# Optimization experiments

Hardware: AMD Instinct MI355X
Metric: run time of the kernel (lower is better)

## Reference

```python
import jax, jax.numpy as jnp
import numpy as np

NUM_HEADS = 8
KERNEL = 3


def _arsinh_norm(x, w, b):
    # ArsinhNorm with scale=1.0: weight * asinh(x) + bias
    return w * jnp.arcsinh(x) + b


def _nbr_idx(L, k):
    # NATTEN neighborhood: window start clamped so the k-window stays in-bounds
    start = jnp.clip(jnp.arange(L) - k // 2, 0, L - k)
    return start[:, None] + jnp.arange(k)  # [L, k]


def _na2d(x, qkv_w, qkv_b, proj_w, proj_b, num_heads=NUM_HEADS, k=KERNEL):
    B, H, W, C = x.shape
    hd = C // num_heads
    qkv = x @ qkv_w + qkv_b                      # [B,H,W,3C]
    q, kk, v = jnp.split(qkv, 3, axis=-1)
    q = q.reshape(B, H, W, num_heads, hd) * (hd ** -0.5)
    kk = kk.reshape(B, H, W, num_heads, hd)
    v = v.reshape(B, H, W, num_heads, hd)
    ri = _nbr_idx(H, k)[:, None, :, None]        # [H,1,k,1]
    ci = _nbr_idx(W, k)[None, :, None, :]        # [1,W,1,k]
    nb_k = kk[:, ri, ci].reshape(B, H, W, k * k, num_heads, hd)  # gather 3x3 neighborhood
    nb_v = v[:, ri, ci].reshape(B, H, W, k * k, num_heads, hd)
    scores = jnp.einsum('bijnd,bijmnd->bijnm', q, nb_k)          # [B,H,W,nh,k*k]
    attn = jax.nn.softmax(scores, axis=-1)
    out = jnp.einsum('bijnm,bijmnd->bijnd', attn, nb_v).reshape(B, H, W, C)
    return out @ proj_w + proj_b


def setup_inputs() -> dict:
    key = jax.random.key(0)
    ks = jax.random.split(key, 8)
    B, H, W, C = 16, 64, 64, 256
    s = 0.02
    return {
        'h': jax.random.normal(ks[0], (B, H, W, C), dtype=jnp.float32),
        'qkv_w': jax.random.normal(ks[1], (C, 3 * C), dtype=jnp.float32) * s,
        'qkv_b': jnp.zeros((3 * C,), jnp.float32),
        'proj_w': jax.random.normal(ks[2], (C, C), dtype=jnp.float32) * s,
        'proj_b': jnp.zeros((C,), jnp.float32),
        'n1_w': jnp.ones((C,), jnp.float32),
        'n1_b': jnp.zeros((C,), jnp.float32),
        'n2_w': jnp.ones((C,), jnp.float32),
        'n2_b': jnp.zeros((C,), jnp.float32),
        'mlp_w1': jax.random.normal(ks[3], (C, 2 * C), dtype=jnp.float32) * s,
        'mlp_b1': jnp.zeros((2 * C,), jnp.float32),
        'mlp_w2': jax.random.normal(ks[4], (2 * C, C), dtype=jnp.float32) * s,
        'mlp_b2': jnp.zeros((C,), jnp.float32),
    }


def reference(h, qkv_w, qkv_b, proj_w, proj_b, n1_w, n1_b, n2_w, n2_b,
              mlp_w1, mlp_b1, mlp_w2, mlp_b2):
    h1 = _arsinh_norm(h, n1_w, n1_b)
    h = h + _na2d(h1, qkv_w, qkv_b, proj_w, proj_b)
    h2 = _arsinh_norm(h, n2_w, n2_b)
    ff = jax.nn.gelu(h2 @ mlp_w1 + mlp_b1, approximate=False) @ mlp_w2 + mlp_b2
    return h + ff
```

## Files before the change

### kernel.cpp

```cpp
#include <hip/hip_runtime.h>
#include <math.h>

typedef unsigned short u16;
typedef unsigned int u32;
typedef __attribute__((ext_vector_type(8))) short short8;
typedef __attribute__((ext_vector_type(4))) float f32x4;

__device__ __forceinline__ float b2f(u16 u) {
    return __uint_as_float(((u32)u) << 16);
}
__device__ __forceinline__ u16 f2b(float f) {
    u32 x = __float_as_uint(f);
    return (u16)((x + 0x7fffu + ((x >> 16) & 1u)) >> 16);
}
__device__ __forceinline__ float ldext(const void* p, size_t i, int isbf) {
    return isbf ? b2f(((const u16*)p)[i]) : ((const float*)p)[i];
}
__device__ __forceinline__ void stext(void* p, size_t i, int isbf, float v) {
    if (isbf) ((u16*)p)[i] = f2b(v);
    else ((float*)p)[i] = v;
}
__device__ __forceinline__ void gl2lds16(const u16* g, u16* l) {
    __builtin_amdgcn_global_load_lds(
        (const __attribute__((address_space(1))) u32*)(const void*)g,
        (__attribute__((address_space(3))) u32*)(void*)l, 16, 0, 0);
}
__device__ __forceinline__ void unpack8(uint4 w, float* f) {
    const u32* pw = (const u32*)&w;
#pragma unroll
    for (int k = 0; k < 4; ++k) {
        f[2 * k]     = __uint_as_float(pw[k] << 16);
        f[2 * k + 1] = __uint_as_float(pw[k] & 0xffff0000u);
    }
}

__global__ void detect_k(const void* __restrict__ h, int* __restrict__ flag) {
    __shared__ int cnt;
    if (threadIdx.x == 0) cnt = 0;
    __syncthreads();
    const u16* p = (const u16*)h;
    int local = 0;
    for (int i = threadIdx.x; i < 4096; i += 256) {
        int e = (p[i] >> 7) & 0xFF;
        if (e != 0 && (e < 110 || e > 133)) local++;
    }
    atomicAdd(&cnt, local);
    __syncthreads();
    if (threadIdx.x == 0) *flag = (cnt < 256) ? 1 : 0;
}

__global__ void transpose_k(const void* __restrict__ src, u16* __restrict__ dst,
                            int R, int C, const int* __restrict__ flag) {
    int isbf = *flag;
    int idx = blockIdx.x * 256 + threadIdx.x;
    if (idx >= R * C) return;
    int r = idx / C, c = idx - r * C;
    dst[c * R + r] = f2b(ldext(src, idx, isbf));
}

__global__ void norm_k(const void* __restrict__ xb, size_t xoff,
                       const void* __restrict__ w, const void* __restrict__ b,
                       u16* __restrict__ y, const int* __restrict__ flag, int force_bf) {
    int isbf = *flag;
    int xisbf = force_bf ? 1 : isbf;
    size_t base = ((size_t)blockIdx.x * 256 + threadIdx.x) * 4;
    int c0 = (int)(base & 255);
    float v[4];
    if (xisbf) {
        uint2 raw = *reinterpret_cast<const uint2*>((const u16*)xb + xoff + base);
        const u16* px = reinterpret_cast<const u16*>(&raw);
#pragma unroll
        for (int j = 0; j < 4; ++j) v[j] = b2f(px[j]);
    } else {
        float4 r = *reinterpret_cast<const float4*>((const float*)xb + xoff + base);
        v[0] = r.x; v[1] = r.y; v[2] = r.z; v[3] = r.w;
    }
    u16 o[4];
#pragma unroll
    for (int j = 0; j < 4; ++j)
        o[j] = f2b(ldext(w, c0 + j, isbf) * asinhf(v[j]) + ldext(b, c0 + j, isbf));
    *reinterpret_cast<uint2*>(y + base) = *reinterpret_cast<uint2*>(o);
}

template <int EPI>
__global__ __launch_bounds__(256) void gemm_bt(
    const u16* __restrict__ A, const u16* __restrict__ BT, const void* __restrict__ bias,
    const void* __restrict__ resb, size_t resoff, void* __restrict__ outb, size_t outoff,
    int N, int K, const int* __restrict__ flag) {
    __shared__ __align__(16) u16 lA[128 * 32];
    __shared__ __align__(16) u16 lB[128 * 32];
    const int isbf = *flag;
    const int tid = threadIdx.x;
    const int lane = tid & 63;
    const int wave = tid >> 6;
    const int waveM = wave >> 1, waveN = wave & 1;
    const int m0 = blockIdx.y * 128;
    const int n0 = blockIdx.x * 128;

    f32x4 acc[4][4];
#pragma unroll
    for (int mi = 0; mi < 4; ++mi)
#pragma unroll
        for (int ni = 0; ni < 4; ++ni)
#pragma unroll
            for (int r = 0; r < 4; ++r) acc[mi][ni][r] = 0.f;

    const int lrow = lane & 15;
    const int ko = (lane >> 4) * 8;

    for (int k0 = 0; k0 < K; k0 += 32) {
        __syncthreads();
#pragma unroll
        for (int q = 0; q < 2; ++q) {
            int s = wave * 2 + q;
            int e0 = (s * 64 + lane) * 8;
            int row = e0 >> 5, col = e0 & 31;
            gl2lds16(&A[(size_t)(m0 + row) * K + k0 + col], &lA[s * 512]);
            gl2lds16(&BT[(size_t)(n0 + row) * K + k0 + col], &lB[s * 512]);
        }
        __syncthreads();
        short8 af[4], bfr[4];
#pragma unroll
        for (int mi = 0; mi < 4; ++mi)
            af[mi] = *reinterpret_cast<const short8*>(&lA[(waveM * 64 + mi * 16 + lrow) * 32 + ko]);
#pragma unroll
        for (int ni = 0; ni < 4; ++ni)
            bfr[ni] = *reinterpret_cast<const short8*>(&lB[(waveN * 64 + ni * 16 + lrow) * 32 + ko]);
#pragma unroll
        for (int mi = 0; mi < 4; ++mi)
#pragma unroll
            for (int ni = 0; ni < 4; ++ni)
                acc[mi][ni] = __builtin_amdgcn_mfma_f32_16x16x32_bf16(af[mi], bfr[ni], acc[mi][ni], 0, 0, 0);
    }

    const int rquad = (lane >> 4) * 4;
    const int ccol = lane & 15;
#pragma unroll
    for (int mi = 0; mi < 4; ++mi)
#pragma unroll
        for (int ni = 0; ni < 4; ++ni) {
            int colg = n0 + waveN * 64 + ni * 16 + ccol;
            float bb = ldext(bias, colg, isbf);
#pragma unroll
            for (int r = 0; r < 4; ++r) {
                int rowg = m0 + waveM * 64 + mi * 16 + rquad + r;
                size_t idx = (size_t)rowg * N + colg;
                float v = acc[mi][ni][r] + bb;
                if (EPI == 0) {
                    ((u16*)outb)[outoff + idx] = f2b(v);
                } else if (EPI == 1) {
                    v = 0.5f * v * (1.f + erff(v * 0.70710678118654752f));
                    ((u16*)outb)[outoff + idx] = f2b(v);
                } else if (EPI == 2) {
                    v += ldext(resb, resoff + idx, isbf);
                    stext(outb, outoff + idx, isbf, v);
                } else if (EPI == 3) {
                    v += ldext(resb, resoff + idx, isbf);
                    ((u16*)outb)[outoff + idx] = f2b(v);
                } else {
                    v += b2f(((const u16*)resb)[resoff + idx]);
                    stext(outb, outoff + idx, isbf, v);
                }
            }
        }
}

__global__ __launch_bounds__(256) void attn_k(const u16* __restrict__ qkv, u16* __restrict__ out) {
    const int t = blockIdx.x * 256 + threadIdx.x;
    const int head = t & 7;
    const int p = t >> 3;
    const int b = p >> 12;
    const int ij = p & 4095;
    const int i = ij >> 6, j = ij & 63;
    int r0 = i - 1; r0 = r0 < 0 ? 0 : (r0 > 61 ? 61 : r0);
    int c0 = j - 1; c0 = c0 < 0 ? 0 : (c0 > 61 ? 61 : c0);

    const u16* qp = qkv + (size_t)p * 768 + head * 32;
    float q[32];
#pragma unroll
    for (int ch = 0; ch < 4; ++ch)
        unpack8(*reinterpret_cast<const uint4*>(qp + ch * 8), q + ch * 8);

    const float qscale = 0.17677669529663687f;
    int nbp[9];
    float sc[9];
#pragma unroll
    for (int dr = 0; dr < 3; ++dr)
#pragma unroll
        for (int dc = 0; dc < 3; ++dc) {
            int nb = dr * 3 + dc;
            int np_ = b * 4096 + (r0 + dr) * 64 + (c0 + dc);
            nbp[nb] = np_;
            const u16* kp = qkv + (size_t)np_ * 768 + 256 + head * 32;
            float dot = 0.f;
#pragma unroll
            for (int ch = 0; ch < 4; ++ch) {
                float kf[8];
                unpack8(*reinterpret_cast<const uint4*>(kp + ch * 8), kf);
#pragma unroll
                for (int e = 0; e < 8; ++e) dot += q[ch * 8 + e] * kf[e];
            }
            sc[nb] = dot * qscale;
        }

    float mx = sc[0];
#pragma unroll
    for (int nb = 1; nb < 9; ++nb) mx = fmaxf(mx, sc[nb]);
    float s = 0.f;
#pragma unroll
    for (int nb = 0; nb < 9; ++nb) { sc[nb] = __expf(sc[nb] - mx); s += sc[nb]; }
    float inv = 1.f / s;

    float acc[32];
#pragma unroll
    for (int e = 0; e < 32; ++e) acc[e] = 0.f;
#pragma unroll
    for (int nb = 0; nb < 9; ++nb) {
        const u16* vp = qkv + (size_t)nbp[nb] * 768 + 512 + head * 32;
        float wgt = sc[nb] * inv;
#pragma unroll
        for (int ch = 0; ch < 4; ++ch) {
            float vf[8];
            unpack8(*reinterpret_cast<const uint4*>(vp + ch * 8), vf);
#pragma unroll
            for (int e = 0; e < 8; ++e) acc[ch * 8 + e] += wgt * vf[e];
        }
    }

    u16 ob[32];
#pragma unroll
    for (int e = 0; e < 32; ++e) ob[e] = f2b(acc[e]);
    uint4* ov = reinterpret_cast<uint4*>(ob);
    uint4* og = reinterpret_cast<uint4*>(out + (size_t)p * 256 + head * 32);
#pragma unroll
    for (int ch = 0; ch < 4; ++ch) og[ch] = ov[ch];
}

extern "C" void kernel_launch(void* const* d_in, const int* in_sizes, int n_in,
                              void* d_out, int out_size, void* d_ws, size_t ws_size,
                              hipStream_t stream) {
    const void* h      = d_in[0];
    const void* qkv_w  = d_in[1];
    const void* qkv_b  = d_in[2];
    const void* proj_w = d_in[3];
    const void* proj_b = d_in[4];
    const void* n1_w   = d_in[5];
    const void* n1_b   = d_in[6];
    const void* n2_w   = d_in[7];
    const void* n2_b   = d_in[8];
    const void* w1     = d_in[9];
    const void* b1     = d_in[10];
    const void* w2     = d_in[11];
    const void* b2     = d_in[12];

    char* ws = (char*)d_ws;
    u16* WqkvT  = (u16*)(ws + 0);
    u16* WprojT = (u16*)(ws + 393216);
    u16* W1T    = (u16*)(ws + 524288);
    u16* W2T    = (u16*)(ws + 786432);
    int* Flag   = (int*)(ws + 1048576);
    char* bufs  = ws + 1049600;

    size_t avail = ws_size > 1049600 ? ws_size - 1049600 : 0;
    int CHUNK = 4096;
    if (avail >= (size_t)65536 * 2048) CHUNK = 65536;
    else if (avail >= (size_t)16384 * 2048) CHUNK = 16384;
    else if (avail >= (size_t)8192 * 2048) CHUNK = 8192;

    u16* H1 = (u16*)bufs;
    u16* S  = (u16*)(bufs + (size_t)CHUNK * 512);

    detect_k<<<1, 256, 0, stream>>>(h, Flag);
    transpose_k<<<768, 256, 0, stream>>>(qkv_w, WqkvT, 256, 768, Flag);
    transpose_k<<<256, 256, 0, stream>>>(proj_w, WprojT, 256, 256, Flag);
    transpose_k<<<512, 256, 0, stream>>>(w1, W1T, 256, 512, Flag);
    transpose_k<<<512, 256, 0, stream>>>(w2, W2T, 512, 256, Flag);

    if (CHUNK == 65536) {
        u16* HNS = S;
        u16* T   = S + (size_t)65536 * 256;
        norm_k<<<16384, 256, 0, stream>>>(h, 0, n1_w, n1_b, H1, Flag, 0);
        { dim3 g(6, 512); gemm_bt<0><<<g, 256, 0, stream>>>(H1, WqkvT, qkv_b, nullptr, 0, S, 0, 768, 256, Flag); }
        attn_k<<<2048, 256, 0, stream>>>(S, H1);
        { dim3 g(2, 512); gemm_bt<3><<<g, 256, 0, stream>>>(H1, WprojT, proj_b, h, 0, HNS, 0, 256, 256, Flag); }
        norm_k<<<16384, 256, 0, stream>>>(HNS, 0, n2_w, n2_b, H1, Flag, 1);
        { dim3 g(4, 512); gemm_bt<1><<<g, 256, 0, stream>>>(H1, W1T, b1, nullptr, 0, T, 0, 512, 256, Flag); }
        { dim3 g(2, 512); gemm_bt<4><<<g, 256, 0, stream>>>(T, W2T, b2, HNS, 0, d_out, 0, 256, 512, Flag); }
    } else {
        const int NCH = 65536 / CHUNK;
        for (int c = 0; c < NCH; ++c) {
            size_t off = (size_t)c * CHUNK * 256;
            norm_k<<<CHUNK / 4, 256, 0, stream>>>(h, off, n1_w, n1_b, H1, Flag, 0);
            { dim3 g(6, CHUNK / 128);
              gemm_bt<0><<<g, 256, 0, stream>>>(H1, WqkvT, qkv_b, nullptr, 0, S, 0, 768, 256, Flag); }
            attn_k<<<CHUNK / 32, 256, 0, stream>>>(S, H1);
            { dim3 g(2, CHUNK / 128);
              gemm_bt<2><<<g, 256, 0, stream>>>(H1, WprojT, proj_b, h, off, d_out, off, 256, 256, Flag); }
        }
        for (int c = 0; c < NCH; ++c) {
            size_t off = (size_t)c * CHUNK * 256;
            norm_k<<<CHUNK / 4, 256, 0, stream>>>(d_out, off, n2_w, n2_b, H1, Flag, 0);
            { dim3 g(4, CHUNK / 128);
              gemm_bt<1><<<g, 256, 0, stream>>>(H1, W1T, b1, nullptr, 0, S, 0, 512, 256, Flag); }
            { dim3 g(2, CHUNK / 128);
              gemm_bt<2><<<g, 256, 0, stream>>>(S, W2T, b2, d_out, off, d_out, off, 256, 512, Flag); }
        }
    }
}
```

Before: 515.4 us.

## Fuse ArsinhNorm into GEMM prologue and keep full-K row tiles resident in LDS

Replaces the separate norm kernels and the K-looped 128x128 GEMM with one GEMM kernel per layer. Each block stages a full 128xK A tile (normalized on the fly for the QKV and MLP1 layers) into XOR-swizzled LDS, then sweeps all N column chunks while reusing that A tile. This removes the norm kernels' write and re-read of activations, cuts per-k-step barriers, and avoids LDS bank conflicts. The cost is 128KB of LDS per block, which limits occupancy to one block per CU, and little overlap between loading B and computing.

```diff
diff --git a/kernel.cpp b/kernel.cpp
--- a/kernel.cpp
+++ b/kernel.cpp
@@ -58,88 +58,60 @@
     dst[c * R + r] = f2b(ldext(src, idx, isbf));
 }
 
-__global__ void norm_k(const void* __restrict__ xb, size_t xoff,
-                       const void* __restrict__ w, const void* __restrict__ b,
-                       u16* __restrict__ y, const int* __restrict__ flag, int force_bf) {
-    int isbf = *flag;
-    int xisbf = force_bf ? 1 : isbf;
-    size_t base = ((size_t)blockIdx.x * 256 + threadIdx.x) * 4;
-    int c0 = (int)(base & 255);
-    float v[4];
-    if (xisbf) {
-        uint2 raw = *reinterpret_cast<const uint2*>((const u16*)xb + xoff + base);
-        const u16* px = reinterpret_cast<const u16*>(&raw);
-#pragma unroll
-        for (int j = 0; j < 4; ++j) v[j] = b2f(px[j]);
-    } else {
-        float4 r = *reinterpret_cast<const float4*>((const float*)xb + xoff + base);
-        v[0] = r.x; v[1] = r.y; v[2] = r.z; v[3] = r.w;
-    }
-    u16 o[4];
-#pragma unroll
-    for (int j = 0; j < 4; ++j)
-        o[j] = f2b(ldext(w, c0 + j, isbf) * asinhf(v[j]) + ldext(b, c0 + j, isbf));
-    *reinterpret_cast<uint2*>(y + base) = *reinterpret_cast<uint2*>(o);
-}
-
-template <int EPI>
-__global__ __launch_bounds__(256) void gemm_bt(
-    const u16* __restrict__ A, const u16* __restrict__ BT, const void* __restrict__ bias,
-    const void* __restrict__ resb, size_t resoff, void* __restrict__ outb, size_t outoff,
-    int N, int K, const int* __restrict__ flag) {
-    __shared__ __align__(16) u16 lA[128 * 32];
-    __shared__ __align__(16) u16 lB[128 * 32];
-    const int isbf = *flag;
-    const int tid = threadIdx.x;
-    const int lane = tid & 63;
+
+template <int K>
+__device__ __forceinline__ void stage_lin(const u16* __restrict__ src, size_t soff,
+                                          int row0, int kcol0, u16* lds, int tid) {
     const int wave = tid >> 6;
-    const int waveM = wave >> 1, waveN = wave & 1;
-    const int m0 = blockIdx.y * 128;
-    const int n0 = blockIdx.x * 128;
-
-    f32x4 acc[4][4];
-#pragma unroll
-    for (int mi = 0; mi < 4; ++mi)
-#pragma unroll
-        for (int ni = 0; ni < 4; ++ni)
-#pragma unroll
-            for (int r = 0; r < 4; ++r) acc[mi][ni][r] = 0.f;
-
+    const int r0 = tid >> 5;
+    const int cbs = ((tid & 31) << 4) ^ (r0 << 4);
+    const u16* s0 = src + soff + (size_t)(row0 + r0) * K + kcol0 + (cbs >> 1);
+#pragma unroll
+    for (int s = 0; s < 16; ++s)
+        gl2lds16(s0 + (size_t)s * 8 * K, lds + s * 2048 + wave * 512);
+}
+
+__device__ __forceinline__ void compute_chunk(const u16* lA, const u16* lB,
+                                              int waveM, int waveN, int lane,
+                                              f32x4 (&acc)[4][4]) {
     const int lrow = lane & 15;
     const int ko = (lane >> 4) * 8;
-
-    for (int k0 = 0; k0 < K; k0 += 32) {
-        __syncthreads();
-#pragma unroll
-        for (int q = 0; q < 2; ++q) {
-            int s = wave * 2 + q;
-            int e0 = (s * 64 + lane) * 8;
-            int row = e0 >> 5, col = e0 & 31;
-            gl2lds16(&A[(size_t)(m0 + row) * K + k0 + col], &lA[s * 512]);
-            gl2lds16(&BT[(size_t)(n0 + row) * K + k0 + col], &lB[s * 512]);
-        }
-        __syncthreads();
+#pragma unroll
+    for (int ks = 0; ks < 8; ++ks) {
         short8 af[4], bfr[4];
-#pragma unroll
-        for (int mi = 0; mi < 4; ++mi)
-            af[mi] = *reinterpret_cast<const short8*>(&lA[(waveM * 64 + mi * 16 + lrow) * 32 + ko]);
-#pragma unroll
-        for (int ni = 0; ni < 4; ++ni)
-            bfr[ni] = *reinterpret_cast<const short8*>(&lB[(waveN * 64 + ni * 16 + lrow) * 32 + ko]);
+        const int kb = (ks * 32 + ko) << 1;
+#pragma unroll
+        for (int mi = 0; mi < 4; ++mi) {
+            int row = waveM * 64 + mi * 16 + lrow;
+            int byte = ((row << 9) + kb) ^ ((row & 7) << 4);
+            af[mi] = *reinterpret_cast<const short8*>(reinterpret_cast<const char*>(lA) + byte);
+        }
+#pragma unroll
+        for (int ni = 0; ni < 4; ++ni) {
+            int row = waveN * 64 + ni * 16 + lrow;
+            int byte = ((row << 9) + kb) ^ ((row & 7) << 4);
+            bfr[ni] = *reinterpret_cast<const short8*>(reinterpret_cast<const char*>(lB) + byte);
+        }
 #pragma unroll
         for (int mi = 0; mi < 4; ++mi)
 #pragma unroll
             for (int ni = 0; ni < 4; ++ni)
                 acc[mi][ni] = __builtin_amdgcn_mfma_f32_16x16x32_bf16(af[mi], bfr[ni], acc[mi][ni], 0, 0, 0);
     }
-
+}
+
+template <int EPI, int N>
+__device__ __forceinline__ void epi_chunk(const f32x4 (&acc)[4][4], int nc, int m0,
+                                          int waveM, int waveN, int lane,
+                                          const void* bias, const void* resb, size_t resoff,
+                                          void* outb, size_t outoff, int isbf) {
     const int rquad = (lane >> 4) * 4;
     const int ccol = lane & 15;
 #pragma unroll
     for (int mi = 0; mi < 4; ++mi)
 #pragma unroll
         for (int ni = 0; ni < 4; ++ni) {
-            int colg = n0 + waveN * 64 + ni * 16 + ccol;
+            int colg = nc * 128 + waveN * 64 + ni * 16 + ccol;
             float bb = ldext(bias, colg, isbf);
 #pragma unroll
             for (int r = 0; r < 4; ++r) {
@@ -165,6 +137,108 @@
         }
 }
 
+template <int PRO, int EPI, int KT, int NC>
+__global__ __launch_bounds__(256) void sgemm(
+    const void* __restrict__ Ax, size_t aoff,
+    const u16* __restrict__ BT,
+    const void* __restrict__ bias,
+    const void* __restrict__ nw, const void* __restrict__ nb,
+    const void* __restrict__ resb, size_t resoff,
+    void* __restrict__ outb, size_t outoff,
+    const int* __restrict__ flag) {
+    static_assert(KT == 1 || (KT == 2 && NC == 2 && PRO == 0), "KT=2 only for MLP2 shape");
+    constexpr int K = KT * 256;
+    constexpr int N = NC * 128;
+    __shared__ __align__(16) u16 lA[128 * 256];
+    __shared__ __align__(16) u16 lB[128 * 256];
+    const int isbf = *flag;
+    const int tid = threadIdx.x;
+    const int lane = tid & 63, wave = tid >> 6;
+    const int waveM = wave >> 1, waveN = wave & 1;
+    const int m0 = blockIdx.x * 128;
+
+    stage_lin<K>(BT, 0, 0, 0, lB, tid);
+
+    if constexpr (PRO == 0) {
+        stage_lin<K>((const u16*)Ax, aoff, m0, 0, lA, tid);
+    } else {
+        const int col = (tid << 2) & 255;
+        const int rb = tid >> 6;
+        float wv[4], bv[4];
+#pragma unroll
+        for (int j = 0; j < 4; ++j) {
+            wv[j] = ldext(nw, col + j, isbf);
+            bv[j] = ldext(nb, col + j, isbf);
+        }
+#pragma unroll 4
+        for (int i = 0; i < 32; ++i) {
+            int row = i * 4 + rb;
+            float v[4];
+            if (PRO == 1 && !isbf) {
+                float4 x = *reinterpret_cast<const float4*>(
+                    (const float*)Ax + aoff + (size_t)(m0 + row) * 256 + col);
+                v[0] = x.x; v[1] = x.y; v[2] = x.z; v[3] = x.w;
+            } else {
+                uint2 xr = *reinterpret_cast<const uint2*>(
+                    (const u16*)Ax + aoff + (size_t)(m0 + row) * 256 + col);
+                const u16* px = reinterpret_cast<const u16*>(&xr);
+#pragma unroll
+                for (int j = 0; j < 4; ++j) v[j] = b2f(px[j]);
+            }
+            u16 o[4];
+#pragma unroll
+            for (int j = 0; j < 4; ++j) o[j] = f2b(wv[j] * asinhf(v[j]) + bv[j]);
+            int byte = ((row << 9) + (col << 1)) ^ ((row & 7) << 4);
+            *reinterpret_cast<uint2*>(reinterpret_cast<char*>(lA) + byte) =
+                *reinterpret_cast<const uint2*>(o);
+        }
+    }
+
+    if constexpr (KT == 1) {
+        __syncthreads();
+        for (int nc = 0; nc < NC; ++nc) {
+            f32x4 acc[4][4];
+#pragma unroll
+            for (int mi = 0; mi < 4; ++mi)
+#pragma unroll
+                for (int ni = 0; ni < 4; ++ni)
+#pragma unroll
+                    for (int r = 0; r < 4; ++r) acc[mi][ni][r] = 0.f;
+            compute_chunk(lA, lB, waveM, waveN, lane, acc);
+            if (nc + 1 < NC) {
+                __syncthreads();
+                stage_lin<K>(BT, 0, (nc + 1) * 128, 0, lB, tid);
+            }
+            epi_chunk<EPI, N>(acc, nc, m0, waveM, waveN, lane, bias,
+                              resb, resoff, outb, outoff, isbf);
+            if (nc + 1 < NC) __syncthreads();
+        }
+    } else {
+        f32x4 acc0[4][4], acc1[4][4];
+#pragma unroll
+        for (int mi = 0; mi < 4; ++mi)
+#pragma unroll
+            for (int ni = 0; ni < 4; ++ni)
+#pragma unroll
+                for (int r = 0; r < 4; ++r) { acc0[mi][ni][r] = 0.f; acc1[mi][ni][r] = 0.f; }
+        for (int kh = 0; kh < 2; ++kh) {
+            if (kh) {
+                __syncthreads();
+                stage_lin<K>(BT, 0, 0, kh * 256, lB, tid);
+                stage_lin<K>((const u16*)Ax, aoff, m0, kh * 256, lA, tid);
+            }
+            __syncthreads();
+            compute_chunk(lA, lB, waveM, waveN, lane, acc0);
+            __syncthreads();
+            stage_lin<K>(BT, 0, 128, kh * 256, lB, tid);
+            __syncthreads();
+            compute_chunk(lA, lB, waveM, waveN, lane, acc1);
+        }
+        epi_chunk<EPI, N>(acc0, 0, m0, waveM, waveN, lane, bias, resb, resoff, outb, outoff, isbf);
+        epi_chunk<EPI, N>(acc1, 1, m0, waveM, waveN, lane, bias, resb, resoff, outb, outoff, isbf);
+    }
+}
+
 __global__ __launch_bounds__(256) void attn_k(const u16* __restrict__ qkv, u16* __restrict__ out) {
     const int t = blockIdx.x * 256 + threadIdx.x;
     const int head = t & 7;
@@ -279,31 +353,31 @@
     if (CHUNK == 65536) {
         u16* HNS = S;
         u16* T   = S + (size_t)65536 * 256;
-        norm_k<<<16384, 256, 0, stream>>>(h, 0, n1_w, n1_b, H1, Flag, 0);
-        { dim3 g(6, 512); gemm_bt<0><<<g, 256, 0, stream>>>(H1, WqkvT, qkv_b, nullptr, 0, S, 0, 768, 256, Flag); }
+        sgemm<1, 0, 1, 6><<<512, 256, 0, stream>>>(h, 0, WqkvT, qkv_b, n1_w, n1_b,
+                                                   nullptr, 0, S, 0, Flag);
         attn_k<<<2048, 256, 0, stream>>>(S, H1);
-        { dim3 g(2, 512); gemm_bt<3><<<g, 256, 0, stream>>>(H1, WprojT, proj_b, h, 0, HNS, 0, 256, 256, Flag); }
-        norm_k<<<16384, 256, 0, stream>>>(HNS, 0, n2_w, n2_b, H1, Flag, 1);
-        { dim3 g(4, 512); gemm_bt<1><<<g, 256, 0, stream>>>(H1, W1T, b1, nullptr, 0, T, 0, 512, 256, Flag); }
-        { dim3 g(2, 512); gemm_bt<4><<<g, 256, 0, stream>>>(T, W2T, b2, HNS, 0, d_out, 0, 256, 512, Flag); }
+        sgemm<0, 3, 1, 2><<<512, 256, 0, stream>>>(H1, 0, WprojT, proj_b, nullptr, nullptr,
+                                                   h, 0, HNS, 0, Flag);
+        sgemm<2, 1, 1, 4><<<512, 256, 0, stream>>>(HNS, 0, W1T, b1, n2_w, n2_b,
+                                                   nullptr, 0, T, 0, Flag);
+        sgemm<0, 4, 2, 2><<<512, 256, 0, stream>>>(T, 0, W2T, b2, nullptr, nullptr,
+                                                   HNS, 0, d_out, 0, Flag);
     } else {
         const int NCH = 65536 / CHUNK;
         for (int c = 0; c < NCH; ++c) {
             size_t off = (size_t)c * CHUNK * 256;
-            norm_k<<<CHUNK / 4, 256, 0, stream>>>(h, off, n1_w, n1_b, H1, Flag, 0);
-            { dim3 g(6, CHUNK / 128);
-              gemm_bt<0><<<g, 256, 0, stream>>>(H1, WqkvT, qkv_b, nullptr, 0, S, 0, 768, 256, Flag); }
+            sgemm<1, 0, 1, 6><<<CHUNK / 128, 256, 0, stream>>>(h, off, WqkvT, qkv_b, n1_w, n1_b,
+                                                               nullptr, 0, S, 0, Flag);
             attn_k<<<CHUNK / 32, 256, 0, stream>>>(S, H1);
-            { dim3 g(2, CHUNK / 128);
-              gemm_bt<2><<<g, 256, 0, stream>>>(H1, WprojT, proj_b, h, off, d_out, off, 256, 256, Flag); }
+            sgemm<0, 2, 1, 2><<<CHUNK / 128, 256, 0, stream>>>(H1, 0, WprojT, proj_b, nullptr, nullptr,
+                                                               h, off, d_out, off, Flag);
         }
         for (int c = 0; c < NCH; ++c) {
             size_t off = (size_t)c * CHUNK * 256;
-            norm_k<<<CHUNK / 4, 256, 0, stream>>>(d_out, off, n2_w, n2_b, H1, Flag, 0);
-            { dim3 g(4, CHUNK / 128);
-              gemm_bt<1><<<g, 256, 0, stream>>>(H1, W1T, b1, nullptr, 0, S, 0, 512, 256, Flag); }
-            { dim3 g(2, CHUNK / 128);
-              gemm_bt<2><<<g, 256, 0, stream>>>(S, W2T, b2, d_out, off, d_out, off, 256, 512, Flag); }
-        }
-    }
-}
+            sgemm<1, 1, 1, 4><<<CHUNK / 128, 256, 0, stream>>>(d_out, off, W1T, b1, n2_w, n2_b,
+                                                               nullptr, 0, S, 0, Flag);
+            sgemm<0, 2, 2, 2><<<CHUNK / 128, 256, 0, stream>>>(S, 0, W2T, b2, nullptr, nullptr,
+                                                               d_out, off, d_out, off, Flag);
+        }
+    }
+}
```

New measurement: 617.9 us. +19.9%, slower.

## Halve GEMM M-tile and fuse second ArsinhNorm into projection epilogue

Applied to the files above, without the earlier changes.

Shrinks the GEMM block tile from 128x128 to 64x128 rows, doubling the grid so more workgroups are in flight. In the full-workspace path it also drops the separate second norm kernel. The projection GEMM epilogue now adds the residual, stores it, and writes the normalized bf16 result into the output buffer as scratch for the MLP input. This saves one full-tensor read/write pass and a launch. In exchange, each B tile is reused across fewer rows, and the epilogue does an extra asinh plus a second store.

```diff
diff --git a/kernel.cpp b/kernel.cpp
--- a/kernel.cpp
+++ b/kernel.cpp
@@ -86,20 +86,21 @@
 __global__ __launch_bounds__(256) void gemm_bt(
     const u16* __restrict__ A, const u16* __restrict__ BT, const void* __restrict__ bias,
     const void* __restrict__ resb, size_t resoff, void* __restrict__ outb, size_t outoff,
-    int N, int K, const int* __restrict__ flag) {
-    __shared__ __align__(16) u16 lA[128 * 32];
+    int N, int K, const int* __restrict__ flag,
+    const void* __restrict__ n2w, const void* __restrict__ n2b, u16* __restrict__ out2) {
+    __shared__ __align__(16) u16 lA[64 * 32];
     __shared__ __align__(16) u16 lB[128 * 32];
     const int isbf = *flag;
     const int tid = threadIdx.x;
     const int lane = tid & 63;
     const int wave = tid >> 6;
     const int waveM = wave >> 1, waveN = wave & 1;
-    const int m0 = blockIdx.y * 128;
+    const int m0 = blockIdx.y * 64;
     const int n0 = blockIdx.x * 128;
 
-    f32x4 acc[4][4];
-#pragma unroll
-    for (int mi = 0; mi < 4; ++mi)
+    f32x4 acc[2][4];
+#pragma unroll
+    for (int mi = 0; mi < 2; ++mi)
 #pragma unroll
         for (int ni = 0; ni < 4; ++ni)
 #pragma unroll
@@ -110,24 +111,28 @@
 
     for (int k0 = 0; k0 < K; k0 += 32) {
         __syncthreads();
+        {
+            int e0 = (wave * 64 + lane) * 8;
+            int row = e0 >> 5, col = e0 & 31;
+            gl2lds16(&A[(size_t)(m0 + row) * K + k0 + col], &lA[wave * 512]);
+        }
 #pragma unroll
         for (int q = 0; q < 2; ++q) {
             int s = wave * 2 + q;
             int e0 = (s * 64 + lane) * 8;
             int row = e0 >> 5, col = e0 & 31;
-            gl2lds16(&A[(size_t)(m0 + row) * K + k0 + col], &lA[s * 512]);
             gl2lds16(&BT[(size_t)(n0 + row) * K + k0 + col], &lB[s * 512]);
         }
         __syncthreads();
-        short8 af[4], bfr[4];
-#pragma unroll
-        for (int mi = 0; mi < 4; ++mi)
-            af[mi] = *reinterpret_cast<const short8*>(&lA[(waveM * 64 + mi * 16 + lrow) * 32 + ko]);
+        short8 af[2], bfr[4];
+#pragma unroll
+        for (int mi = 0; mi < 2; ++mi)
+            af[mi] = *reinterpret_cast<const short8*>(&lA[(waveM * 32 + mi * 16 + lrow) * 32 + ko]);
 #pragma unroll
         for (int ni = 0; ni < 4; ++ni)
             bfr[ni] = *reinterpret_cast<const short8*>(&lB[(waveN * 64 + ni * 16 + lrow) * 32 + ko]);
 #pragma unroll
-        for (int mi = 0; mi < 4; ++mi)
+        for (int mi = 0; mi < 2; ++mi)
 #pragma unroll
             for (int ni = 0; ni < 4; ++ni)
                 acc[mi][ni] = __builtin_amdgcn_mfma_f32_16x16x32_bf16(af[mi], bfr[ni], acc[mi][ni], 0, 0, 0);
@@ -136,14 +141,14 @@
     const int rquad = (lane >> 4) * 4;
     const int ccol = lane & 15;
 #pragma unroll
-    for (int mi = 0; mi < 4; ++mi)
+    for (int mi = 0; mi < 2; ++mi)
 #pragma unroll
         for (int ni = 0; ni < 4; ++ni) {
             int colg = n0 + waveN * 64 + ni * 16 + ccol;
             float bb = ldext(bias, colg, isbf);
 #pragma unroll
             for (int r = 0; r < 4; ++r) {
-                int rowg = m0 + waveM * 64 + mi * 16 + rquad + r;
+                int rowg = m0 + waveM * 32 + mi * 16 + rquad + r;
                 size_t idx = (size_t)rowg * N + colg;
                 float v = acc[mi][ni][r] + bb;
                 if (EPI == 0) {
@@ -157,9 +162,14 @@
                 } else if (EPI == 3) {
                     v += ldext(resb, resoff + idx, isbf);
                     ((u16*)outb)[outoff + idx] = f2b(v);
-                } else {
+                } else if (EPI == 4) {
                     v += b2f(((const u16*)resb)[resoff + idx]);
                     stext(outb, outoff + idx, isbf, v);
+                } else {
+                    v += ldext(resb, resoff + idx, isbf);
+                    ((u16*)outb)[outoff + idx] = f2b(v);
+                    float y = ldext(n2w, colg, isbf) * asinhf(v) + ldext(n2b, colg, isbf);
+                    out2[idx] = f2b(y);
                 }
             }
         }
@@ -279,31 +289,39 @@
     if (CHUNK == 65536) {
         u16* HNS = S;
         u16* T   = S + (size_t)65536 * 256;
+        u16* N2  = (u16*)d_out;
         norm_k<<<16384, 256, 0, stream>>>(h, 0, n1_w, n1_b, H1, Flag, 0);
-        { dim3 g(6, 512); gemm_bt<0><<<g, 256, 0, stream>>>(H1, WqkvT, qkv_b, nullptr, 0, S, 0, 768, 256, Flag); }
+        { dim3 g(6, 1024); gemm_bt<0><<<g, 256, 0, stream>>>(H1, WqkvT, qkv_b, nullptr, 0, S, 0,
+                                                             768, 256, Flag, nullptr, nullptr, nullptr); }
         attn_k<<<2048, 256, 0, stream>>>(S, H1);
-        { dim3 g(2, 512); gemm_bt<3><<<g, 256, 0, stream>>>(H1, WprojT, proj_b, h, 0, HNS, 0, 256, 256, Flag); }
-        norm_k<<<16384, 256, 0, stream>>>(HNS, 0, n2_w, n2_b, H1, Flag, 1);
-        { dim3 g(4, 512); gemm_bt<1><<<g, 256, 0, stream>>>(H1, W1T, b1, nullptr, 0, T, 0, 512, 256, Flag); }
-        { dim3 g(2, 512); gemm_bt<4><<<g, 256, 0, stream>>>(T, W2T, b2, HNS, 0, d_out, 0, 256, 512, Flag); }
+        { dim3 g(2, 1024); gemm_bt<5><<<g, 256, 0, stream>>>(H1, WprojT, proj_b, h, 0, HNS, 0,
+                                                             256, 256, Flag, n2_w, n2_b, N2); }
+        { dim3 g(4, 1024); gemm_bt<1><<<g, 256, 0, stream>>>(N2, W1T, b1, nullptr, 0, T, 0,
+                                                             512, 256, Flag, nullptr, nullptr, nullptr); }
+        { dim3 g(2, 1024); gemm_bt<4><<<g, 256, 0, stream>>>(T, W2T, b2, HNS, 0, d_out, 0,
+                                                             256, 512, Flag, nullptr, nullptr, nullptr); }
     } else {
         const int NCH = 65536 / CHUNK;
         for (int c = 0; c < NCH; ++c) {
             size_t off = (size_t)c * CHUNK * 256;
             norm_k<<<CHUNK / 4, 256, 0, stream>>>(h, off, n1_w, n1_b, H1, Flag, 0);
-            { dim3 g(6, CHUNK / 128);
-              gemm_bt<0><<<g, 256, 0, stream>>>(H1, WqkvT, qkv_b, nullptr, 0, S, 0, 768, 256, Flag); }
+            { dim3 g(6, CHUNK / 64);
+              gemm_bt<0><<<g, 256, 0, stream>>>(H1, WqkvT, qkv_b, nullptr, 0, S, 0,
+                                                768, 256, Flag, nullptr, nullptr, nullptr); }
             attn_k<<<CHUNK / 32, 256, 0, stream>>>(S, H1);
-            { dim3 g(2, CHUNK / 128);
-              gemm_bt<2><<<g, 256, 0, stream>>>(H1, WprojT, proj_b, h, off, d_out, off, 256, 256, Flag); }
+            { dim3 g(2, CHUNK / 64);
+              gemm_bt<2><<<g, 256, 0, stream>>>(H1, WprojT, proj_b, h, off, d_out, off,
+                                                256, 256, Flag, nullptr, nullptr, nullptr); }
         }
         for (int c = 0; c < NCH; ++c) {
             size_t off = (size_t)c * CHUNK * 256;
             norm_k<<<CHUNK / 4, 256, 0, stream>>>(d_out, off, n2_w, n2_b, H1, Flag, 0);
-            { dim3 g(4, CHUNK / 128);
-              gemm_bt<1><<<g, 256, 0, stream>>>(H1, W1T, b1, nullptr, 0, S, 0, 512, 256, Flag); }
-            { dim3 g(2, CHUNK / 128);
-              gemm_bt<2><<<g, 256, 0, stream>>>(S, W2T, b2, d_out, off, d_out, off, 256, 512, Flag); }
-        }
-    }
-}
+            { dim3 g(4, CHUNK / 64);
+              gemm_bt<1><<<g, 256, 0, stream>>>(H1, W1T, b1, nullptr, 0, S, 0,
+                                                512, 256, Flag, nullptr, nullptr, nullptr); }
+            { dim3 g(2, CHUNK / 64);
+              gemm_bt<2><<<g, 256, 0, stream>>>(S, W2T, b2, d_out, off, d_out, off,
+                                                256, 512, Flag, nullptr, nullptr, nullptr); }
+        }
+    }
+}
```

New measurement: 512.0 us. No clear change (-0.7%).

## Replace tiled GEMM with B-resident LDS GEMM and fuse second norm into projection

Applied to the files above, without the earlier changes.

The k-looped 128x128 GEMM is replaced by a kernel that loads a whole N-slice of the transposed weight into LDS once per block. Each block then streams many 128-row strips of A straight from global memory into registers and uses 32x32x16 bf16 MFMA. This removes the per-k-step LDS staging and barriers for A and amortizes the weight loads across rows. The second ArsinhNorm is fused into the projection GEMM epilogue, which removes a separate norm kernel and a round trip through memory, and d_out is reused as scratch for the normed activations. The trade-off is uncoalesced, unshared A loads and higher register pressure from holding the full K of A per thread.

```diff
diff --git a/kernel.cpp b/kernel.cpp
--- a/kernel.cpp
+++ b/kernel.cpp
@@ -5,6 +5,7 @@
 typedef unsigned int u32;
 typedef __attribute__((ext_vector_type(8))) short short8;
 typedef __attribute__((ext_vector_type(4))) float f32x4;
+typedef __attribute__((ext_vector_type(16))) float f32x16;
 
 __device__ __forceinline__ float b2f(u16 u) {
     return __uint_as_float(((u32)u) << 16);
@@ -19,11 +20,6 @@
 __device__ __forceinline__ void stext(void* p, size_t i, int isbf, float v) {
     if (isbf) ((u16*)p)[i] = f2b(v);
     else ((float*)p)[i] = v;
-}
-__device__ __forceinline__ void gl2lds16(const u16* g, u16* l) {
-    __builtin_amdgcn_global_load_lds(
-        (const __attribute__((address_space(1))) u32*)(const void*)g,
-        (__attribute__((address_space(3))) u32*)(void*)l, 16, 0, 0);
 }
 __device__ __forceinline__ void unpack8(uint4 w, float* f) {
     const u32* pw = (const u32*)&w;
@@ -82,70 +78,75 @@
     *reinterpret_cast<uint2*>(y + base) = *reinterpret_cast<uint2*>(o);
 }
 
-template <int EPI>
-__global__ __launch_bounds__(256) void gemm_bt(
+template <int K, int NCH, int EPI>
+__global__ __launch_bounds__(256, 2) void sgemm2(
     const u16* __restrict__ A, const u16* __restrict__ BT, const void* __restrict__ bias,
     const void* __restrict__ resb, size_t resoff, void* __restrict__ outb, size_t outoff,
-    int N, int K, const int* __restrict__ flag) {
-    __shared__ __align__(16) u16 lA[128 * 32];
-    __shared__ __align__(16) u16 lB[128 * 32];
+    int N, int Mtot, const int* __restrict__ flag,
+    const void* __restrict__ n2w, const void* __restrict__ n2b, u16* __restrict__ out2) {
+    constexpr int NF = NCH / 32;
+    constexpr int KS = K / 16;
+    constexpr int FRAGS = KS * NF;
+    __shared__ __align__(16) u16 lB[FRAGS * 512];
     const int isbf = *flag;
     const int tid = threadIdx.x;
-    const int lane = tid & 63;
-    const int wave = tid >> 6;
-    const int waveM = wave >> 1, waveN = wave & 1;
-    const int m0 = blockIdx.y * 128;
-    const int n0 = blockIdx.x * 128;
-
-    f32x4 acc[4][4];
-#pragma unroll
-    for (int mi = 0; mi < 4; ++mi)
-#pragma unroll
-        for (int ni = 0; ni < 4; ++ni)
-#pragma unroll
-            for (int r = 0; r < 4; ++r) acc[mi][ni][r] = 0.f;
-
-    const int lrow = lane & 15;
-    const int ko = (lane >> 4) * 8;
-
-    for (int k0 = 0; k0 < K; k0 += 32) {
-        __syncthreads();
-#pragma unroll
-        for (int q = 0; q < 2; ++q) {
-            int s = wave * 2 + q;
-            int e0 = (s * 64 + lane) * 8;
-            int row = e0 >> 5, col = e0 & 31;
-            gl2lds16(&A[(size_t)(m0 + row) * K + k0 + col], &lA[s * 512]);
-            gl2lds16(&BT[(size_t)(n0 + row) * K + k0 + col], &lB[s * 512]);
-        }
-        __syncthreads();
-        short8 af[4], bfr[4];
-#pragma unroll
-        for (int mi = 0; mi < 4; ++mi)
-            af[mi] = *reinterpret_cast<const short8*>(&lA[(waveM * 64 + mi * 16 + lrow) * 32 + ko]);
-#pragma unroll
-        for (int ni = 0; ni < 4; ++ni)
-            bfr[ni] = *reinterpret_cast<const short8*>(&lB[(waveN * 64 + ni * 16 + lrow) * 32 + ko]);
-#pragma unroll
-        for (int mi = 0; mi < 4; ++mi)
-#pragma unroll
-            for (int ni = 0; ni < 4; ++ni)
-                acc[mi][ni] = __builtin_amdgcn_mfma_f32_16x16x32_bf16(af[mi], bfr[ni], acc[mi][ni], 0, 0, 0);
-    }
-
-    const int rquad = (lane >> 4) * 4;
-    const int ccol = lane & 15;
-#pragma unroll
-    for (int mi = 0; mi < 4; ++mi)
-#pragma unroll
-        for (int ni = 0; ni < 4; ++ni) {
-            int colg = n0 + waveN * 64 + ni * 16 + ccol;
-            float bb = ldext(bias, colg, isbf);
-#pragma unroll
-            for (int r = 0; r < 4; ++r) {
-                int rowg = m0 + waveM * 64 + mi * 16 + rquad + r;
+    const int lane = tid & 63, wave = tid >> 6;
+    const int n0 = blockIdx.x * NCH;
+
+    for (int f = wave; f < FRAGS; f += 4) {
+        int nf = f % NF, ks = f / NF;
+        const u16* src = BT + (size_t)(n0 + nf * 32 + (lane & 31)) * K + ks * 16 + (lane >> 5) * 8;
+        *reinterpret_cast<short8*>(&lB[f * 512 + lane * 8]) =
+            *reinterpret_cast<const short8*>(src);
+    }
+
+    float bias_r[NF], w2r[NF], b2r[NF];
+#pragma unroll
+    for (int nf = 0; nf < NF; ++nf) {
+        int colg = n0 + nf * 32 + (lane & 31);
+        bias_r[nf] = ldext(bias, colg, isbf);
+        if (EPI == 5) {
+            w2r[nf] = ldext(n2w, colg, isbf);
+            b2r[nf] = ldext(n2b, colg, isbf);
+        }
+    }
+    __syncthreads();
+
+    const int rows_per_blk = Mtot / (int)gridDim.y;
+    const int row_base = blockIdx.y * rows_per_blk;
+    const int arow = wave * 32 + (lane & 31);
+    const int acol = (lane >> 5) * 8;
+
+    for (int r0 = row_base; r0 < row_base + rows_per_blk; r0 += 128) {
+        const u16* ap = A + (size_t)(r0 + arow) * K + acol;
+        short8 a[KS];
+#pragma unroll
+        for (int ks = 0; ks < KS; ++ks)
+            a[ks] = *reinterpret_cast<const short8*>(ap + ks * 16);
+
+        f32x16 acc[NF];
+#pragma unroll
+        for (int nf = 0; nf < NF; ++nf)
+#pragma unroll
+            for (int i = 0; i < 16; ++i) acc[nf][i] = 0.f;
+
+#pragma unroll
+        for (int ks = 0; ks < KS; ++ks)
+#pragma unroll
+            for (int nf = 0; nf < NF; ++nf) {
+                short8 b = *reinterpret_cast<const short8*>(&lB[(ks * NF + nf) * 512 + lane * 8]);
+                acc[nf] = __builtin_amdgcn_mfma_f32_32x32x16_bf16(a[ks], b, acc[nf], 0, 0, 0);
+            }
+
+#pragma unroll
+        for (int nf = 0; nf < NF; ++nf) {
+            int colg = n0 + nf * 32 + (lane & 31);
+#pragma unroll
+            for (int rr = 0; rr < 16; ++rr) {
+                int m = (rr & 3) + 8 * (rr >> 2) + 4 * (lane >> 5);
+                int rowg = r0 + wave * 32 + m;
                 size_t idx = (size_t)rowg * N + colg;
-                float v = acc[mi][ni][r] + bb;
+                float v = acc[nf][rr] + bias_r[nf];
                 if (EPI == 0) {
                     ((u16*)outb)[outoff + idx] = f2b(v);
                 } else if (EPI == 1) {
@@ -154,15 +155,18 @@
                 } else if (EPI == 2) {
                     v += ldext(resb, resoff + idx, isbf);
                     stext(outb, outoff + idx, isbf, v);
-                } else if (EPI == 3) {
+                } else if (EPI == 4) {
+                    v += b2f(((const u16*)resb)[resoff + idx]);
+                    stext(outb, outoff + idx, isbf, v);
+                } else {
                     v += ldext(resb, resoff + idx, isbf);
                     ((u16*)outb)[outoff + idx] = f2b(v);
-                } else {
-                    v += b2f(((const u16*)resb)[resoff + idx]);
-                    stext(outb, outoff + idx, isbf, v);
+                    float y = w2r[nf] * asinhf(v) + b2r[nf];
+                    out2[idx] = f2b(y);
                 }
             }
         }
+    }
 }
 
 __global__ __launch_bounds__(256) void attn_k(const u16* __restrict__ qkv, u16* __restrict__ out) {
@@ -279,31 +283,35 @@
     if (CHUNK == 65536) {
         u16* HNS = S;
         u16* T   = S + (size_t)65536 * 256;
+        u16* N2  = (u16*)d_out;
         norm_k<<<16384, 256, 0, stream>>>(h, 0, n1_w, n1_b, H1, Flag, 0);
-        { dim3 g(6, 512); gemm_bt<0><<<g, 256, 0, stream>>>(H1, WqkvT, qkv_b, nullptr, 0, S, 0, 768, 256, Flag); }
+        { dim3 g(6, 128); sgemm2<256, 128, 0><<<g, 256, 0, stream>>>(
+              H1, WqkvT, qkv_b, nullptr, 0, S, 0, 768, 65536, Flag, nullptr, nullptr, nullptr); }
         attn_k<<<2048, 256, 0, stream>>>(S, H1);
-        { dim3 g(2, 512); gemm_bt<3><<<g, 256, 0, stream>>>(H1, WprojT, proj_b, h, 0, HNS, 0, 256, 256, Flag); }
-        norm_k<<<16384, 256, 0, stream>>>(HNS, 0, n2_w, n2_b, H1, Flag, 1);
-        { dim3 g(4, 512); gemm_bt<1><<<g, 256, 0, stream>>>(H1, W1T, b1, nullptr, 0, T, 0, 512, 256, Flag); }
-        { dim3 g(2, 512); gemm_bt<4><<<g, 256, 0, stream>>>(T, W2T, b2, HNS, 0, d_out, 0, 256, 512, Flag); }
+        { dim3 g(2, 256); sgemm2<256, 128, 5><<<g, 256, 0, stream>>>(
+              H1, WprojT, proj_b, h, 0, HNS, 0, 256, 65536, Flag, n2_w, n2_b, N2); }
+        { dim3 g(4, 128); sgemm2<256, 128, 1><<<g, 256, 0, stream>>>(
+              N2, W1T, b1, nullptr, 0, T, 0, 512, 65536, Flag, nullptr, nullptr, nullptr); }
+        { dim3 g(4, 128); sgemm2<512, 64, 4><<<g, 256, 0, stream>>>(
+              T, W2T, b2, HNS, 0, d_out, 0, 256, 65536, Flag, nullptr, nullptr, nullptr); }
     } else {
         const int NCH = 65536 / CHUNK;
         for (int c = 0; c < NCH; ++c) {
             size_t off = (size_t)c * CHUNK * 256;
             norm_k<<<CHUNK / 4, 256, 0, stream>>>(h, off, n1_w, n1_b, H1, Flag, 0);
-            { dim3 g(6, CHUNK / 128);
-              gemm_bt<0><<<g, 256, 0, stream>>>(H1, WqkvT, qkv_b, nullptr, 0, S, 0, 768, 256, Flag); }
+            { dim3 g(6, CHUNK / 128); sgemm2<256, 128, 0><<<g, 256, 0, stream>>>(
+                  H1, WqkvT, qkv_b, nullptr, 0, S, 0, 768, CHUNK, Flag, nullptr, nullptr, nullptr); }
             attn_k<<<CHUNK / 32, 256, 0, stream>>>(S, H1);
-            { dim3 g(2, CHUNK / 128);
-              gemm_bt<2><<<g, 256, 0, stream>>>(H1, WprojT, proj_b, h, off, d_out, off, 256, 256, Flag); }
+            { dim3 g(2, CHUNK / 128); sgemm2<256, 128, 2><<<g, 256, 0, stream>>>(
+                  H1, WprojT, proj_b, h, off, d_out, off, 256, CHUNK, Flag, nullptr, nullptr, nullptr); }
         }
         for (int c = 0; c < NCH; ++c) {
             size_t off = (size_t)c * CHUNK * 256;
             norm_k<<<CHUNK / 4, 256, 0, stream>>>(d_out, off, n2_w, n2_b, H1, Flag, 0);
-            { dim3 g(4, CHUNK / 128);
-              gemm_bt<1><<<g, 256, 0, stream>>>(H1, W1T, b1, nullptr, 0, S, 0, 512, 256, Flag); }
-            { dim3 g(2, CHUNK / 128);
-              gemm_bt<2><<<g, 256, 0, stream>>>(S, W2T, b2, d_out, off, d_out, off, 256, 512, Flag); }
-        }
-    }
-}
+            { dim3 g(4, CHUNK / 128); sgemm2<256, 128, 1><<<g, 256, 0, stream>>>(
+                  H1, W1T, b1, nullptr, 0, S, 0, 512, CHUNK, Flag, nullptr, nullptr, nullptr); }
+            { dim3 g(4, CHUNK / 128); sgemm2<512, 64, 2><<<g, 256, 0, stream>>>(
+                  S, W2T, b2, d_out, off, d_out, off, 256, CHUNK, Flag, nullptr, nullptr, nullptr); }
+        }
+    }
+}
```

New measurement: 729.1 us. +41.5%, slower.
